# Kernel tuning notes

Measured on AMD Instinct MI355X. Metric: run time of the kernel, lower is better.

Reference implementation:

```python
import jax, jax.numpy as jnp
import numpy as np

FP16_HUGE = 2.0 ** 15
NUM_HEAD = 4
LN_EPS = 1e-5


def setup_inputs() -> dict:
    key = jax.random.key(0)
    ks = jax.random.split(key, 12)
    B, N, D = 1, 256, 128
    H = NUM_HEAD
    inp = {
        "pair_act": jax.random.normal(ks[0], (B, N, N, D), dtype=jnp.float32),
        "pair_mask": jnp.ones((B, N, N), dtype=jnp.float32),
        "ln_scale": jnp.ones((D,), dtype=jnp.float32),
        "ln_bias": jnp.zeros((D,), dtype=jnp.float32),
        # torch Linear weight layout: [out_dim, in_dim]; applied as x @ W.T
        "w2d": jax.random.normal(ks[1], (H, D), dtype=jnp.float32) / np.sqrt(D),
        "wq": jax.random.normal(ks[2], (D, D), dtype=jnp.float32) / np.sqrt(D),
        "wk": jax.random.normal(ks[3], (D, D), dtype=jnp.float32) / np.sqrt(D),
        "wv": jax.random.normal(ks[4], (D, D), dtype=jnp.float32) / np.sqrt(D),
        "wg": jax.random.normal(ks[5], (D, D), dtype=jnp.float32) / np.sqrt(D),
        "bg": jnp.ones((D,), dtype=jnp.float32),  # gating bias init = 1.0
        "wo": jax.random.normal(ks[6], (D, D), dtype=jnp.float32) * 0.02,
        "bo": jnp.zeros((D,), dtype=jnp.float32),
    }
    return inp


def reference(pair_act, pair_mask, ln_scale, ln_bias, w2d, wq, wk, wv, wg, bg, wo, bo):
    B, N, _, D = pair_act.shape
    H = NUM_HEAD
    kd = D // H  # per-head key/value dim
    scale = kd ** (-0.5)

    # mask bias: [B, N(row), 1, 1, N(key)]
    bias = (FP16_HUGE * (pair_mask - 1.0))[:, :, None, None, :]

    # LayerNorm (fp32, eps=1e-5)
    mu = jnp.mean(pair_act, axis=-1, keepdims=True)
    var = jnp.mean(jnp.square(pair_act - mu), axis=-1, keepdims=True)
    x = (pair_act - mu) * jax.lax.rsqrt(var + LN_EPS) * ln_scale + ln_bias

    # non-batched per-head bias: [B, 1, H, N, N]
    nb = jnp.einsum("bijd,hd->bhij", x, w2d)[:, None]

    q = (x @ wq.T).reshape(B, N, N, H, kd) * scale  # [B, r, i, H, kd]
    k = (x @ wk.T).reshape(B, N, N, H, kd)
    v = (x @ wv.T).reshape(B, N, N, H, kd)

    logits = jnp.einsum("brihk,brjhk->brhij", q, k) + bias + nb  # [B, r, H, i, j]
    w = jax.nn.softmax(logits, axis=-1)
    o = jnp.einsum("brhij,brjhv->brihv", w, v)  # [B, r, i, H, kd]

    g = jax.nn.sigmoid(x @ wg.T + bg).reshape(B, N, N, H, kd)
    o = (o * g).reshape(B, N, N, D)

    out = o @ wo.T + bo
    return out * pair_mask[..., None]
```

## Files before the change

### kernel.cpp

```cpp
#include <hip/hip_runtime.h>
#include <hip/hip_bf16.h>

typedef unsigned short u16;
typedef __attribute__((ext_vector_type(8))) short bf16x8;
typedef __attribute__((ext_vector_type(4))) float f32x4;
typedef __attribute__((address_space(3))) unsigned lds_u32;
typedef const __attribute__((address_space(1))) unsigned glb_u32;

#define N 256
#define D 128
#define NH 4
#define KD 32
#define NN 65536
#define QK_SCALE 0.17677669529663687f
#define LOG2E 1.4426950408889634f
#define HUGE_MASK 32768.0f

__device__ __forceinline__ float b2f(u16 s) {
  union { float f; unsigned u; } x; x.u = ((unsigned)s) << 16; return x.f;
}
__device__ __forceinline__ u16 f2b(float f) {
  union { float f; unsigned u; } x; x.f = f;
  unsigned r = x.u + 0x7fff + ((x.u >> 16) & 1);
  return (u16)(r >> 16);
}
__device__ __forceinline__ float exp2v(float x) {
  float r; __asm__("v_exp_f32 %0, %1" : "=v"(r) : "v"(x)); return r;
}

__global__ __launch_bounds__(256) void prep_w_kernel(
    const float* __restrict__ wq, const float* __restrict__ wk,
    const float* __restrict__ wv, const float* __restrict__ wg,
    const float* __restrict__ wo, u16* __restrict__ wb)
{
  int idx = blockIdx.x * 256 + threadIdx.x;
  const float* srcs[5] = {wq, wk, wv, wg, wo};
  int mat = idx >> 11, rem = idx & 2047;
  int row = rem >> 4, g = rem & 15;
  int gp = (g + (row & 15)) & 15;
  const float* s = srcs[mat] + row * 128 + g * 8;
  float4 f0 = *(const float4*)(s);
  float4 f1 = *(const float4*)(s + 4);
  uint4 pk;
  pk.x = (unsigned)f2b(f0.x) | ((unsigned)f2b(f0.y) << 16);
  pk.y = (unsigned)f2b(f0.z) | ((unsigned)f2b(f0.w) << 16);
  pk.z = (unsigned)f2b(f1.x) | ((unsigned)f2b(f1.y) << 16);
  pk.w = (unsigned)f2b(f1.z) | ((unsigned)f2b(f1.w) << 16);
  *(uint4*)(wb + (size_t)mat * 16384 + row * 128 + gp * 8) = pk;
}

template <int CPW>
__device__ __forceinline__ void stage_lin(const u16* __restrict__ gsrc, u16* lds, int tid) {
  int lane = tid & 63, wave = tid >> 6;
#pragma unroll
  for (int p = 0; p < CPW; p++) {
    int c = wave * CPW + p;
    __builtin_amdgcn_global_load_lds((glb_u32*)(gsrc + c * 512 + lane * 8),
                                     (lds_u32*)(lds + c * 512), 16, 0, 0);
  }
}

__global__ __launch_bounds__(512) void projln_kernel(
    const float* __restrict__ pa, const float* __restrict__ lns, const float* __restrict__ lnb,
    const float* __restrict__ w2d, const u16* __restrict__ wb, const float* __restrict__ bg,
    u16* __restrict__ q, u16* __restrict__ kf, u16* __restrict__ vf, u16* __restrict__ g,
    float* __restrict__ nb)
{
  __shared__ __align__(16) u16 Wl[2][16384];
  int tid = threadIdx.x;
  int wave = tid >> 6, lane = tid & 63;
  int lr = lane & 15, quad = lane >> 4;

  stage_lin<4>(wb, Wl[0], tid);

  bf16x8 a[4];
  int row = blockIdx.x * 128 + wave * 16 + lr;
  {
    const float* rp = pa + (size_t)row * D;
    float xv[4][8];
    float s = 0.f, ss = 0.f;
#pragma unroll
    for (int ks = 0; ks < 4; ks++) {
      float4 a0 = *(const float4*)(rp + ks * 32 + quad * 8);
      float4 a1 = *(const float4*)(rp + ks * 32 + quad * 8 + 4);
      xv[ks][0] = a0.x; xv[ks][1] = a0.y; xv[ks][2] = a0.z; xv[ks][3] = a0.w;
      xv[ks][4] = a1.x; xv[ks][5] = a1.y; xv[ks][6] = a1.z; xv[ks][7] = a1.w;
#pragma unroll
      for (int j = 0; j < 8; j++) { s += xv[ks][j]; ss += xv[ks][j] * xv[ks][j]; }
    }
    s  += __shfl_xor(s, 16, 64);  ss += __shfl_xor(ss, 16, 64);
    s  += __shfl_xor(s, 32, 64);  ss += __shfl_xor(ss, 32, 64);
    float mu = s * (1.0f / D);
    float var = ss * (1.0f / D) - mu * mu;
    float rs = rsqrtf(var + 1e-5f);
#pragma unroll
    for (int ks = 0; ks < 4; ks++) {
      float4 s0 = *(const float4*)(lns + ks * 32 + quad * 8);
      float4 s1 = *(const float4*)(lns + ks * 32 + quad * 8 + 4);
      float4 b0 = *(const float4*)(lnb + ks * 32 + quad * 8);
      float4 b1 = *(const float4*)(lnb + ks * 32 + quad * 8 + 4);
      float sc[8] = {s0.x,s0.y,s0.z,s0.w,s1.x,s1.y,s1.z,s1.w};
      float bi[8] = {b0.x,b0.y,b0.z,b0.w,b1.x,b1.y,b1.z,b1.w};
#pragma unroll
      for (int j = 0; j < 8; j++) xv[ks][j] = (xv[ks][j] - mu) * rs * sc[j] + bi[j];
    }
#pragma unroll
    for (int h = 0; h < NH; h++) {
      float p = 0.f;
#pragma unroll
      for (int ks = 0; ks < 4; ks++) {
        float4 w0 = *(const float4*)(w2d + h * D + ks * 32 + quad * 8);
        float4 w1 = *(const float4*)(w2d + h * D + ks * 32 + quad * 8 + 4);
        p += xv[ks][0]*w0.x + xv[ks][1]*w0.y + xv[ks][2]*w0.z + xv[ks][3]*w0.w
           + xv[ks][4]*w1.x + xv[ks][5]*w1.y + xv[ks][6]*w1.z + xv[ks][7]*w1.w;
      }
      p += __shfl_xor(p, 16, 64);
      p += __shfl_xor(p, 32, 64);
      if (quad == 0)
        nb[(size_t)h * NN + row] = p * LOG2E;
    }
#pragma unroll
    for (int ks = 0; ks < 4; ks++)
#pragma unroll
      for (int j = 0; j < 8; j++) a[ks][j] = (short)f2b(xv[ks][j]);
  }
  __syncthreads();

#pragma unroll
  for (int mat = 0; mat < 4; mat++) {
    if (mat < 3) stage_lin<4>(wb + (size_t)(mat + 1) * 16384, Wl[(mat + 1) & 1], tid);
    const u16* Wcur = Wl[mat & 1];
    f32x4 acc[2][4];
#pragma unroll
    for (int tg = 0; tg < 2; tg++)
#pragma unroll
      for (int e = 0; e < 4; e++) acc[tg][e] = (f32x4){0.f, 0.f, 0.f, 0.f};
#pragma unroll
    for (int ks = 0; ks < 4; ks++) {
#pragma unroll
      for (int tg = 0; tg < 2; tg++) {
#pragma unroll
        for (int e = 0; e < 4; e++) {
          int nrow = tg * 64 + 4 * lr + e;
          int gp = (ks * 4 + quad + (nrow & 15)) & 15;
          bf16x8 b = *(const bf16x8*)(&Wcur[nrow * 128 + gp * 8]);
          acc[tg][e] = __builtin_amdgcn_mfma_f32_16x16x32_bf16(a[ks], b, acc[tg][e], 0, 0, 0);
        }
      }
    }
    int row0 = blockIdx.x * 128 + wave * 16 + quad * 4;
#pragma unroll
    for (int tg = 0; tg < 2; tg++) {
      int c0 = tg * 64 + 4 * lr;
      float bg0 = 0.f, bg1 = 0.f, bg2 = 0.f, bg3 = 0.f;
      if (mat == 3) { bg0 = bg[c0]; bg1 = bg[c0+1]; bg2 = bg[c0+2]; bg3 = bg[c0+3]; }
#pragma unroll
      for (int reg = 0; reg < 4; reg++) {
        float v0 = acc[tg][0][reg], v1 = acc[tg][1][reg];
        float v2 = acc[tg][2][reg], v3 = acc[tg][3][reg];
        if (mat == 0) {
          v0 *= QK_SCALE * LOG2E; v1 *= QK_SCALE * LOG2E;
          v2 *= QK_SCALE * LOG2E; v3 *= QK_SCALE * LOG2E;
        }
        if (mat == 3) {
          v0 = 1.0f / (1.0f + __expf(-(v0 + bg0)));
          v1 = 1.0f / (1.0f + __expf(-(v1 + bg1)));
          v2 = 1.0f / (1.0f + __expf(-(v2 + bg2)));
          v3 = 1.0f / (1.0f + __expf(-(v3 + bg3)));
        }
        int R = row0 + reg;
        if (mat == 1) {
          int rr = R >> 8, j = R & 255;
          int t = j >> 4, lrj = j & 15;
          int h2 = c0 >> 5, cc = c0 & 31, qc = cc >> 3, s2 = cc & 7;
          uint2 pk;
          pk.x = (unsigned)f2b(v0) | ((unsigned)f2b(v1) << 16);
          pk.y = (unsigned)f2b(v2) | ((unsigned)f2b(v3) << 16);
          *(uint2*)(kf + (size_t)(rr * NH + h2) * 8192 +
                    ((t * 4 + qc) * 16 + lrj) * 8 + s2) = pk;
        } else if (mat == 2) {
          int rr = R >> 8, j = R & 255;
          int ks2 = j >> 5, jrel = j & 31;
          int qv = (jrel & 15) >> 2;
          int jv = (jrel & 3) | ((jrel >> 4) << 2);
          int h2 = c0 >> 5, cc = c0 & 31;
          size_t base = (size_t)(rr * NH + h2) * 8192;
          u16 vs[4] = {f2b(v0), f2b(v1), f2b(v2), f2b(v3)};
#pragma unroll
          for (int i2 = 0; i2 < 4; i2++) {
            int c = cc + i2, e = c & 1, l = c >> 1;
            vf[base + (((ks2 * 2 + e) * 4 + qv) * 16 + l) * 8 + jv] = vs[i2];
          }
        } else {
          u16* O = (mat == 0) ? q : g;
          uint2 pk;
          pk.x = (unsigned)f2b(v0) | ((unsigned)f2b(v1) << 16);
          pk.y = (unsigned)f2b(v2) | ((unsigned)f2b(v3) << 16);
          *(uint2*)(O + (size_t)R * D + c0) = pk;
        }
      }
    }
    __syncthreads();
  }
}

__global__ __launch_bounds__(512) void attn_kernel(
    const u16* __restrict__ q, const u16* __restrict__ kf, const u16* __restrict__ vf,
    const u16* __restrict__ g, const float* __restrict__ nb, const float* __restrict__ mask,
    u16* __restrict__ og)
{
  __shared__ __align__(16) u16 Kf[8192];
  __shared__ __align__(16) u16 Vf[8192];
  __shared__ float bias_lds[256];
  int h = blockIdx.x & 3, r = blockIdx.x >> 2;
  int tid = threadIdx.x;
  stage_lin<2>(kf + (size_t)(r * NH + h) * 8192, Kf, tid);
  stage_lin<2>(vf + (size_t)(r * NH + h) * 8192, Vf, tid);
  if (tid < 256) bias_lds[tid] = (HUGE_MASK * LOG2E) * (mask[r * N + tid] - 1.0f);
  __syncthreads();

  int wave = tid >> 6, lane = tid & 63;
  int lr = lane & 15, quad = lane >> 4;
  const float* nbh = nb + (size_t)h * NN;

  for (int pp = 0; pp < 2; pp++) {
    int i0 = pp * 128 + wave * 16;
    int irow = i0 + lr;
    bf16x8 af = *(const bf16x8*)(q + ((size_t)r * N + irow) * D + h * KD + quad * 8);
    const float* nbrow = nbh + (size_t)irow * N;
    float m = 0.f, ls = 0.f;
    f32x4 oa = (f32x4){0.f,0.f,0.f,0.f}, ob = (f32x4){0.f,0.f,0.f,0.f};
#pragma unroll 1
    for (int c = 0; c < 2; c++) {
      f32x4 S[8];
#pragma unroll
      for (int tt = 0; tt < 8; tt++) {
        int t = c * 8 + tt;
        int jb = t * 16 + quad * 4;
        float4 nb4 = *(const float4*)(nbrow + jb);
        float4 b4  = *(const float4*)(&bias_lds[jb]);
        f32x4 ci;
        ci[0] = nb4.x + b4.x; ci[1] = nb4.y + b4.y;
        ci[2] = nb4.z + b4.z; ci[3] = nb4.w + b4.w;
        bf16x8 kfr = *(const bf16x8*)(&Kf[((t * 4 + quad) * 16 + lr) * 8]);
        S[tt] = __builtin_amdgcn_mfma_f32_16x16x32_bf16(kfr, af, ci, 0, 0, 0);
      }
      float m0 = -3e38f, m1 = -3e38f, m2 = -3e38f, m3 = -3e38f;
#pragma unroll
      for (int tt = 0; tt < 8; tt++) {
        m0 = fmaxf(m0, S[tt][0]); m1 = fmaxf(m1, S[tt][1]);
        m2 = fmaxf(m2, S[tt][2]); m3 = fmaxf(m3, S[tt][3]);
      }
      float ma = fmaxf(fmaxf(m0, m1), fmaxf(m2, m3));
      ma = fmaxf(ma, __shfl_xor(ma, 16, 64));
      ma = fmaxf(ma, __shfl_xor(ma, 32, 64));
      if (c == 0) {
        m = ma;
      } else {
        float mnew = fmaxf(m, ma);
        float sc = exp2v(m - mnew);
        m = mnew;
        ls *= sc;
        float s0 = __shfl(sc, quad * 4 + 0, 64);
        float s1 = __shfl(sc, quad * 4 + 1, 64);
        float s2 = __shfl(sc, quad * 4 + 2, 64);
        float s3 = __shfl(sc, quad * 4 + 3, 64);
        oa[0] *= s0; oa[1] *= s1; oa[2] *= s2; oa[3] *= s3;
        ob[0] *= s0; ob[1] *= s1; ob[2] *= s2; ob[3] *= s3;
      }
#pragma unroll
      for (int kk = 0; kk < 4; kk++) {
        int ks = c * 4 + kk;
        float p0 = exp2v(S[2*kk][0] - m);
        float p1 = exp2v(S[2*kk][1] - m);
        float p2 = exp2v(S[2*kk][2] - m);
        float p3 = exp2v(S[2*kk][3] - m);
        float p4 = exp2v(S[2*kk+1][0] - m);
        float p5 = exp2v(S[2*kk+1][1] - m);
        float p6 = exp2v(S[2*kk+1][2] - m);
        float p7 = exp2v(S[2*kk+1][3] - m);
        ls += ((p0 + p1) + (p2 + p3)) + ((p4 + p5) + (p6 + p7));
        union { bf16x8 v; unsigned u[4]; } pa;
        __asm__("v_cvt_pk_bf16_f32 %0, %1, %2" : "=v"(pa.u[0]) : "v"(p0), "v"(p1));
        __asm__("v_cvt_pk_bf16_f32 %0, %1, %2" : "=v"(pa.u[1]) : "v"(p2), "v"(p3));
        __asm__("v_cvt_pk_bf16_f32 %0, %1, %2" : "=v"(pa.u[2]) : "v"(p4), "v"(p5));
        __asm__("v_cvt_pk_bf16_f32 %0, %1, %2" : "=v"(pa.u[3]) : "v"(p6), "v"(p7));
        bf16x8 vb0 = *(const bf16x8*)(&Vf[(((ks * 2 + 0) * 4 + quad) * 16 + lr) * 8]);
        oa = __builtin_amdgcn_mfma_f32_16x16x32_bf16(pa.v, vb0, oa, 0, 0, 0);
        bf16x8 vb1 = *(const bf16x8*)(&Vf[(((ks * 2 + 1) * 4 + quad) * 16 + lr) * 8]);
        ob = __builtin_amdgcn_mfma_f32_16x16x32_bf16(pa.v, vb1, ob, 0, 0, 0);
      }
    }
    float lsum = ls;
    lsum += __shfl_xor(lsum, 16, 64);
    lsum += __shfl_xor(lsum, 32, 64);
    float invd = __builtin_amdgcn_rcpf(lsum);

#pragma unroll
    for (int reg = 0; reg < 4; reg++) {
      float inv = __shfl(invd, quad * 4 + reg, 64);
      int i = i0 + quad * 4 + reg;
      size_t base = ((size_t)r * N + i) * D + h * KD + 2 * lr;
      unsigned gv = *(const unsigned*)(g + base);
      float r0 = oa[reg] * inv * b2f((u16)(gv & 0xffff));
      float r1 = ob[reg] * inv * b2f((u16)(gv >> 16));
      *(unsigned*)(og + base) = (unsigned)f2b(r0) | ((unsigned)f2b(r1) << 16);
    }
  }
}

__global__ __launch_bounds__(512) void out_kernel(
    const u16* __restrict__ og, const u16* __restrict__ wob, const float* __restrict__ bo,
    const float* __restrict__ mask, float* __restrict__ out)
{
  __shared__ __align__(16) u16 Wlds[16384];
  int tid = threadIdx.x;
  stage_lin<4>(wob, Wlds, tid);
  int wave = tid >> 6, lane = tid & 63;
  int lr = lane & 15, quad = lane >> 4;
  bf16x8 a[4];
  int arow = blockIdx.x * 128 + wave * 16 + lr;
#pragma unroll
  for (int ks = 0; ks < 4; ks++)
    a[ks] = *(const bf16x8*)(og + (size_t)arow * D + ks * 32 + quad * 8);
  __syncthreads();
  f32x4 acc[2][4];
#pragma unroll
  for (int tg = 0; tg < 2; tg++)
#pragma unroll
    for (int e = 0; e < 4; e++) acc[tg][e] = (f32x4){0.f, 0.f, 0.f, 0.f};
#pragma unroll
  for (int ks = 0; ks < 4; ks++) {
#pragma unroll
    for (int tg = 0; tg < 2; tg++) {
#pragma unroll
      for (int e = 0; e < 4; e++) {
        int nrow = tg * 64 + 4 * lr + e;
        int gp = (ks * 4 + quad + (nrow & 15)) & 15;
        bf16x8 b = *(const bf16x8*)(&Wlds[nrow * 128 + gp * 8]);
        acc[tg][e] = __builtin_amdgcn_mfma_f32_16x16x32_bf16(a[ks], b, acc[tg][e], 0, 0, 0);
      }
    }
  }
  int row0 = blockIdx.x * 128 + wave * 16 + quad * 4;
#pragma unroll
  for (int tg = 0; tg < 2; tg++) {
    int c0 = tg * 64 + 4 * lr;
    float4 bo4 = *(const float4*)(bo + c0);
#pragma unroll
    for (int reg = 0; reg < 4; reg++) {
      int pos = row0 + reg;
      float mk = mask[pos];
      float4 o4;
      o4.x = (acc[tg][0][reg] + bo4.x) * mk;
      o4.y = (acc[tg][1][reg] + bo4.y) * mk;
      o4.z = (acc[tg][2][reg] + bo4.z) * mk;
      o4.w = (acc[tg][3][reg] + bo4.w) * mk;
      *(float4*)(out + (size_t)pos * D + c0) = o4;
    }
  }
}

extern "C" void kernel_launch(void* const* d_in, const int* in_sizes, int n_in,
                              void* d_out, int out_size, void* d_ws, size_t ws_size,
                              hipStream_t stream)
{
  const float* pa   = (const float*)d_in[0];
  const float* mask = (const float*)d_in[1];
  const float* lns  = (const float*)d_in[2];
  const float* lnb  = (const float*)d_in[3];
  const float* w2d  = (const float*)d_in[4];
  const float* wq   = (const float*)d_in[5];
  const float* wk   = (const float*)d_in[6];
  const float* wv   = (const float*)d_in[7];
  const float* wg   = (const float*)d_in[8];
  const float* bg   = (const float*)d_in[9];
  const float* wo   = (const float*)d_in[10];
  const float* bo   = (const float*)d_in[11];

  const size_t ARR = (size_t)NN * D;
  u16* q  = (u16*)d_ws;
  u16* kf = q + ARR;
  u16* vf = kf + ARR;
  u16* g  = vf + ARR;
  u16* og = g + ARR;
  float* nb = (float*)(og + ARR);
  u16* wb = (u16*)(nb + (size_t)NH * NN);

  prep_w_kernel<<<40, 256, 0, stream>>>(wq, wk, wv, wg, wo, wb);
  projln_kernel<<<512, 512, 0, stream>>>(pa, lns, lnb, w2d, wb, bg, q, kf, vf, g, nb);
  attn_kernel<<<N * NH, 512, 0, stream>>>(q, kf, vf, g, nb, mask, og);
  out_kernel<<<512, 512, 0, stream>>>(og, wb + 4 * 16384, bo, mask, (float*)d_out);
}
```

Baseline: 187.6 us.

## Drop LDS staging in attention, read K/V from global, halve block sizes

The attention kernel no longer stages K and V tiles and the mask bias into shared memory. It reads K/V fragments directly from global memory (served by cache) and computes the mask bias inline, which removes the block-wide staging and barrier. Blocks shrink to 256 threads, with twice as many blocks each covering half the query rows, and the output kernel is likewise halved to 256 threads and 1024 blocks. The trade-off is repeated global and L2 reads of K/V per wave and more re-staging of the weight matrix in the output kernel.

```diff
diff --git a/kernel.cpp b/kernel.cpp
--- a/kernel.cpp
+++ b/kernel.cpp
@@ -204,27 +204,24 @@
   }
 }
 
-__global__ __launch_bounds__(512) void attn_kernel(
+__global__ __launch_bounds__(256) void attn_kernel(
     const u16* __restrict__ q, const u16* __restrict__ kf, const u16* __restrict__ vf,
     const u16* __restrict__ g, const float* __restrict__ nb, const float* __restrict__ mask,
     u16* __restrict__ og)
 {
-  __shared__ __align__(16) u16 Kf[8192];
-  __shared__ __align__(16) u16 Vf[8192];
-  __shared__ float bias_lds[256];
-  int h = blockIdx.x & 3, r = blockIdx.x >> 2;
+  int h = blockIdx.x & 3, half = (blockIdx.x >> 2) & 1, r = blockIdx.x >> 3;
   int tid = threadIdx.x;
-  stage_lin<2>(kf + (size_t)(r * NH + h) * 8192, Kf, tid);
-  stage_lin<2>(vf + (size_t)(r * NH + h) * 8192, Vf, tid);
-  if (tid < 256) bias_lds[tid] = (HUGE_MASK * LOG2E) * (mask[r * N + tid] - 1.0f);
-  __syncthreads();
-
   int wave = tid >> 6, lane = tid & 63;
   int lr = lane & 15, quad = lane >> 4;
+  const u16* kfp = kf + (size_t)(r * NH + h) * 8192;
+  const u16* vfp = vf + (size_t)(r * NH + h) * 8192;
   const float* nbh = nb + (size_t)h * NN;
-
+  const float* maskr = mask + r * N;
+  const float CB = HUGE_MASK * LOG2E;
+
+#pragma unroll 1
   for (int pp = 0; pp < 2; pp++) {
-    int i0 = pp * 128 + wave * 16;
+    int i0 = half * 128 + pp * 64 + wave * 16;
     int irow = i0 + lr;
     bf16x8 af = *(const bf16x8*)(q + ((size_t)r * N + irow) * D + h * KD + quad * 8);
     const float* nbrow = nbh + (size_t)irow * N;
@@ -238,11 +235,13 @@
         int t = c * 8 + tt;
         int jb = t * 16 + quad * 4;
         float4 nb4 = *(const float4*)(nbrow + jb);
-        float4 b4  = *(const float4*)(&bias_lds[jb]);
+        float4 m4  = *(const float4*)(maskr + jb);
         f32x4 ci;
-        ci[0] = nb4.x + b4.x; ci[1] = nb4.y + b4.y;
-        ci[2] = nb4.z + b4.z; ci[3] = nb4.w + b4.w;
-        bf16x8 kfr = *(const bf16x8*)(&Kf[((t * 4 + quad) * 16 + lr) * 8]);
+        ci[0] = nb4.x + CB * (m4.x - 1.0f);
+        ci[1] = nb4.y + CB * (m4.y - 1.0f);
+        ci[2] = nb4.z + CB * (m4.z - 1.0f);
+        ci[3] = nb4.w + CB * (m4.w - 1.0f);
+        bf16x8 kfr = *(const bf16x8*)(kfp + (size_t)(t * 64 + lane) * 8);
         S[tt] = __builtin_amdgcn_mfma_f32_16x16x32_bf16(kfr, af, ci, 0, 0, 0);
       }
       float m0 = -3e38f, m1 = -3e38f, m2 = -3e38f, m3 = -3e38f;
@@ -285,9 +284,9 @@
         __asm__("v_cvt_pk_bf16_f32 %0, %1, %2" : "=v"(pa.u[1]) : "v"(p2), "v"(p3));
         __asm__("v_cvt_pk_bf16_f32 %0, %1, %2" : "=v"(pa.u[2]) : "v"(p4), "v"(p5));
         __asm__("v_cvt_pk_bf16_f32 %0, %1, %2" : "=v"(pa.u[3]) : "v"(p6), "v"(p7));
-        bf16x8 vb0 = *(const bf16x8*)(&Vf[(((ks * 2 + 0) * 4 + quad) * 16 + lr) * 8]);
+        bf16x8 vb0 = *(const bf16x8*)(vfp + (size_t)((ks * 2 + 0) * 64 + lane) * 8);
         oa = __builtin_amdgcn_mfma_f32_16x16x32_bf16(pa.v, vb0, oa, 0, 0, 0);
-        bf16x8 vb1 = *(const bf16x8*)(&Vf[(((ks * 2 + 1) * 4 + quad) * 16 + lr) * 8]);
+        bf16x8 vb1 = *(const bf16x8*)(vfp + (size_t)((ks * 2 + 1) * 64 + lane) * 8);
         ob = __builtin_amdgcn_mfma_f32_16x16x32_bf16(pa.v, vb1, ob, 0, 0, 0);
       }
     }
@@ -309,17 +308,17 @@
   }
 }
 
-__global__ __launch_bounds__(512) void out_kernel(
+__global__ __launch_bounds__(256) void out_kernel(
     const u16* __restrict__ og, const u16* __restrict__ wob, const float* __restrict__ bo,
     const float* __restrict__ mask, float* __restrict__ out)
 {
   __shared__ __align__(16) u16 Wlds[16384];
   int tid = threadIdx.x;
-  stage_lin<4>(wob, Wlds, tid);
+  stage_lin<8>(wob, Wlds, tid);
   int wave = tid >> 6, lane = tid & 63;
   int lr = lane & 15, quad = lane >> 4;
   bf16x8 a[4];
-  int arow = blockIdx.x * 128 + wave * 16 + lr;
+  int arow = blockIdx.x * 64 + wave * 16 + lr;
 #pragma unroll
   for (int ks = 0; ks < 4; ks++)
     a[ks] = *(const bf16x8*)(og + (size_t)arow * D + ks * 32 + quad * 8);
@@ -342,7 +341,7 @@
       }
     }
   }
-  int row0 = blockIdx.x * 128 + wave * 16 + quad * 4;
+  int row0 = blockIdx.x * 64 + wave * 16 + quad * 4;
 #pragma unroll
   for (int tg = 0; tg < 2; tg++) {
     int c0 = tg * 64 + 4 * lr;
@@ -389,6 +388,6 @@
 
   prep_w_kernel<<<40, 256, 0, stream>>>(wq, wk, wv, wg, wo, wb);
   projln_kernel<<<512, 512, 0, stream>>>(pa, lns, lnb, w2d, wb, bg, q, kf, vf, g, nb);
-  attn_kernel<<<N * NH, 512, 0, stream>>>(q, kf, vf, g, nb, mask, og);
-  out_kernel<<<512, 512, 0, stream>>>(og, wb + 4 * 16384, bo, mask, (float*)d_out);
-}
+  attn_kernel<<<N * NH * 2, 256, 0, stream>>>(q, kf, vf, g, nb, mask, og);
+  out_kernel<<<1024, 256, 0, stream>>>(og, wb + 4 * 16384, bo, mask, (float*)d_out);
+}
```

Result: slower. 198.8 us (+6.0%).
